# Performance work log

Measured on AMD Instinct MI355X. Metric: run time of the kernel, lower is better.

The kernel has to match this reference:

```python
import jax, jax.numpy as jnp
import numpy as np

POOL_K = {56: 8, 28: 4, 14: 2, 7: 1}


def _maxpool(x, k):
    # kernel == stride maxpool via reshape-max
    if k == 1:
        return x
    B, C, H, W = x.shape
    return x.reshape(B, C, H // k, k, W // k, k).max(axis=(3, 5))


def _scale(act):
    # act: [B, C, H0, W0] -> pooled [B, C, 7, 7]
    B, C, H0, W0 = act.shape
    p = _maxpool(act, POOL_K[H0]).reshape(B, C, -1)  # [B, C, HW], HW=49
    # heatmap[i,j,e,f] = sum_c p[i,c,e] * p[j,c,f]  -> [B, B, HW, HW]
    heat = jax.nn.softmax(jnp.einsum('ice,jcf->ijef', p, p), axis=-1)
    # out[i,j,e,c] = sum_f heat[i,j,e,f] * p[j,c,f]  -> [B, B, HW, C]
    out = jnp.einsum('ijef,jcf->ijec', heat, p)
    return out, heat


def setup_inputs() -> dict:
    key = jax.random.key(0)
    k1, k2, k3, k4 = jax.random.split(key, 4)
    B = 16
    return {
        'act1': jax.random.normal(k1, (B, 256, 56, 56), dtype=jnp.float32),
        'act2': jax.random.normal(k2, (B, 512, 28, 28), dtype=jnp.float32),
        'act3': jax.random.normal(k3, (B, 1024, 14, 14), dtype=jnp.float32),
        'act4': jax.random.normal(k4, (B, 2048, 7, 7), dtype=jnp.float32),
    }


def reference(act1, act2, act3, act4):
    outs_heats = [_scale(a) for a in (act1, act2, act3, act4)]
    outs = tuple(o for o, _ in outs_heats)
    heats = tuple(h for _, h in outs_heats)
    return outs + heats
```

## Files before the change

kernel.cpp:

```cpp
#include <hip/hip_runtime.h>
#include <hip/hip_bf16.h>
#include <cstdint>
#include <cstddef>


typedef __attribute__((ext_vector_type(8))) short s16x8;
typedef __attribute__((ext_vector_type(4))) float f32x4;
typedef __attribute__((ext_vector_type(4))) uint32_t u32x4;

#define SPART 802816

__device__ __forceinline__ unsigned short f2bf(float x) {
    uint32_t u = __float_as_uint(x);
    uint32_t r = (u + 0x7fff + ((u >> 16) & 1)) >> 16;
    return (unsigned short)r;
}
__device__ __forceinline__ float bf2f(unsigned short b) {
    return __uint_as_float(((uint32_t)b) << 16);
}
__device__ __forceinline__ void gll16(const void* g, void* l) {
    __builtin_amdgcn_global_load_lds(
        (const __attribute__((address_space(1))) uint32_t*)g,
        (__attribute__((address_space(3))) uint32_t*)l, 16, 0, 0);
}

struct PoolParams {
    const float* act[4];
    unsigned short* Pk[4];
    unsigned short* Vb[4];
    int C[4], H[4], k[4], G[4], cum[5];
};

__global__ __launch_bounds__(256) void pool_all_kernel(PoolParams pp) {
    __shared__ alignas(16) float plane[3136];
    int b = blockIdx.x, s = 0;
    while (b >= pp.cum[s + 1]) s++;
    const int rem = b - pp.cum[s];
    const int C = pp.C[s], H = pp.H[s], k = pp.k[s], G = pp.G[s];
    const int HW = H * H;
    const int nblk_c = C / G;
    const int i  = rem / nblk_c;
    const int c0 = (rem % nblk_c) * G;
    unsigned short* __restrict__ Pk = pp.Pk[s];
    unsigned short* __restrict__ Vb = pp.Vb[s];

    const float4* src4 = reinterpret_cast<const float4*>(pp.act[s] + ((size_t)i * C + c0) * HW);
    float4* plane4 = reinterpret_cast<float4*>(plane);
    for (int idx = threadIdx.x; idx < (G * HW) >> 2; idx += 256)
        plane4[idx] = src4[idx];
    __syncthreads();
    for (int idx = threadIdx.x; idx < G * 49; idx += 256) {
        const int e = idx / G, g = idx % G;
        const int eh = e / 7, ew = e % 7;
        const float* ppl = plane + g * HW + (eh * k) * H + ew * k;
        float m = -INFINITY;
        for (int dy = 0; dy < k; ++dy)
            for (int dx = 0; dx < k; ++dx)
                m = fmaxf(m, ppl[dy * H + dx]);
        const int c = c0 + g;
        const unsigned short hb = f2bf(m);
        const unsigned short lb = f2bf(m - bf2f(hb));
        const size_t pk = (((size_t)(c >> 2) * 896) + (size_t)i * 56 + e) * 8 + ((c & 3) * 2);
        *reinterpret_cast<uint32_t*>(&Pk[pk]) = (uint32_t)hb | ((uint32_t)lb << 16);
        const size_t vb = (((size_t)i * 8 + (e >> 3)) * C + c) * 8 + (e & 7);
        Vb[vb] = hb;
    }
    for (int idx = threadIdx.x; idx < 7 * G; idx += 256) {
        const int e = 49 + idx / G, g = idx % G, c = c0 + g;
        const size_t pk = (((size_t)(c >> 2) * 896) + (size_t)i * 56 + e) * 8 + ((c & 3) * 2);
        *reinterpret_cast<uint32_t*>(&Pk[pk]) = 0;
    }
    for (int idx = threadIdx.x; idx < 15 * G; idx += 256) {
        const int e = 49 + idx / G, g = idx % G, c = c0 + g;
        const size_t vb = (((size_t)i * 8 + (e >> 3)) * C + c) * 8 + (e & 7);
        Vb[vb] = 0;
    }
}

struct GramParams {
    const unsigned short* Pk[4];
    float* S[4];
    int Kblk[4];
    int cum[5];
};

__global__ __launch_bounds__(256) void gram_kernel(GramParams g) {
    __shared__ short lsA[4 * 128 * 8];
    __shared__ short lsB[4 * 128 * 8];
    int b = blockIdx.x, s = 0;
    while (b >= g.cum[s + 1]) s++;
    const int rem = b - g.cum[s];
    const int p = rem / 49, t = rem % 49;
    const int bi = t / 7, bj = t % 7;
    const int Kb = g.Kblk[s];
    const int kg0 = p * (Kb >> 3);
    const unsigned short* __restrict__ Pk = g.Pk[s];
    float* __restrict__ S = g.S[s] + (size_t)p * SPART;

    const int tid = threadIdx.x, lane = tid & 63, w = tid >> 6;
    const int wm = (w >> 1) * 64, wn = (w & 1) * 64;

    f32x4 acc[4][4];
    #pragma unroll
    for (int u = 0; u < 4; ++u)
        #pragma unroll
        for (int v = 0; v < 4; ++v)
            acc[u][v] = (f32x4){0.f, 0.f, 0.f, 0.f};

    const int half = lane >> 4, r16 = lane & 15;
    for (int it = 0; it < (Kb >> 5); ++it) {
        const int kq = kg0 + it * 4 + w;
        const char* ga = (const char*)Pk + ((size_t)kq * 896 + bi * 128) * 16 + lane * 16;
        const char* gb = (const char*)Pk + ((size_t)kq * 896 + bj * 128) * 16 + lane * 16;
        gll16(ga,        (char*)lsA + w * 2048);
        gll16(ga + 1024, (char*)lsA + w * 2048 + 1024);
        gll16(gb,        (char*)lsB + w * 2048);
        gll16(gb + 1024, (char*)lsB + w * 2048 + 1024);
        __syncthreads();
        s16x8 av[4], bv[4], cv[4];
        #pragma unroll
        for (int u = 0; u < 4; ++u) {
            av[u] = *reinterpret_cast<const s16x8*>(&lsA[((half * 128) + wm + 16 * u + r16) * 8]);
            union { u32x4 u4; s16x8 s8; } ub, uc;
            ub.u4 = *reinterpret_cast<const u32x4*>(&lsB[((half * 128) + wn + 16 * u + r16) * 8]);
            uc.u4 = (ub.u4 >> 16) | (ub.u4 << 16);
            bv[u] = ub.s8;
            cv[u] = uc.s8;
        }
        #pragma unroll
        for (int u = 0; u < 4; ++u)
            #pragma unroll
            for (int v = 0; v < 4; ++v) {
                acc[u][v] = __builtin_amdgcn_mfma_f32_16x16x32_bf16(av[u], bv[v], acc[u][v], 0, 0, 0);
                acc[u][v] = __builtin_amdgcn_mfma_f32_16x16x32_bf16(av[u], cv[v], acc[u][v], 0, 0, 0);
            }
        __syncthreads();
    }

    const int rowb = bi * 128 + wm + (lane >> 4) * 4;
    const int colb = bj * 128 + wn + (lane & 15);
    #pragma unroll
    for (int u = 0; u < 4; ++u)
        #pragma unroll
        for (int v = 0; v < 4; ++v)
            #pragma unroll
            for (int rg = 0; rg < 4; ++rg)
                S[(size_t)(rowb + 16 * u + rg) * 896 + colb + 16 * v] = acc[u][v][rg];
}

struct SoftParams {
    const float* S[4];
    float* heat[4];
    unsigned short* Hb[4];
    int np[4];
};

__global__ __launch_bounds__(256) void softmax_kernel(SoftParams sp) {
    const int grp = (blockIdx.x * 256 + threadIdx.x) >> 4;
    const int l = threadIdx.x & 15;
    const int s = grp / 12544;
    const int rem = grp % 12544;
    const int i = rem / 784;
    const int j = (rem / 49) % 16;
    const int e = rem % 49;
    const float* __restrict__ Sb = sp.S[s];
    const int np = sp.np[s];
    const size_t rowoff = ((size_t)(i * 56 + e)) * 896 + j * 56;

    float v[4];
    #pragma unroll
    for (int t = 0; t < 4; ++t) {
        const int f = l + t * 16;
        float x = -INFINITY;
        if (f < 49) {
            x = 0.f;
            for (int p = 0; p < np; ++p) x += Sb[(size_t)p * SPART + rowoff + f];
        }
        v[t] = x;
    }
    float m = fmaxf(fmaxf(v[0], v[1]), fmaxf(v[2], v[3]));
    #pragma unroll
    for (int d = 1; d < 16; d <<= 1) m = fmaxf(m, __shfl_xor(m, d, 16));
    float ex[4], sum = 0.f;
    #pragma unroll
    for (int t = 0; t < 4; ++t) {
        const int f = l + t * 16;
        ex[t] = (f < 49) ? __expf(v[t] - m) : 0.f;
        sum += ex[t];
    }
    #pragma unroll
    for (int d = 1; d < 16; d <<= 1) sum += __shfl_xor(sum, d, 16);
    const float inv = 1.f / sum;

    float* hrow = sp.heat[s] + (((size_t)(i * 16 + j)) * 49 + e) * 49;
    unsigned short* __restrict__ Hb = sp.Hb[s];
    const size_t hbrow = (size_t)i * 56 + e;
    #pragma unroll
    for (int t = 0; t < 4; ++t) {
        const int f = l + t * 16;
        const float hv = (f < 49) ? ex[t] * inv : 0.f;
        if (f < 49) hrow[f] = hv;
        Hb[(((size_t)j * 8 + (f >> 3)) * 896 + hbrow) * 8 + (f & 7)] = f2bf(hv);
    }
}

struct PvParams {
    const unsigned short* Hb[4];
    const unsigned short* Vb[4];
    float* out[4];
    int C[4];
    int cum[5];
};

__global__ __launch_bounds__(256) void pv_kernel(PvParams pv) {
    __shared__ short lsA[8 * 128 * 8];
    __shared__ short lsB[8 * 128 * 8];
    int b = blockIdx.x, s = 0;
    while (b >= pv.cum[s + 1]) s++;
    int rem = b - pv.cum[s];
    const int C = pv.C[s], nct = C >> 7;
    const int j  = rem / (nct * 2); rem %= nct * 2;
    const int ct = rem >> 1, rh = rem & 1;
    const int tid = threadIdx.x, lane = tid & 63, w = tid >> 6;
    const int wm = (w >> 1) * 64, wn = (w & 1) * 64;
    const unsigned short* __restrict__ Hb = pv.Hb[s];
    const unsigned short* __restrict__ Vb = pv.Vb[s];

    #pragma unroll
    for (int q = 0; q < 2; ++q) {
        const int kq = w + q * 4;
        const char* gb = (const char*)Vb + ((size_t)(j * 8 + kq) * C + ct * 128) * 16 + lane * 16;
        gll16(gb,        (char*)lsB + kq * 2048);
        gll16(gb + 1024, (char*)lsB + kq * 2048 + 1024);
    }

    const int r16 = lane & 15;
    for (int rt = rh; rt < 7; rt += 2) {
        #pragma unroll
        for (int q = 0; q < 2; ++q) {
            const int kq = w + q * 4;
            const char* ga = (const char*)Hb + ((size_t)(j * 8 + kq) * 896 + rt * 128) * 16 + lane * 16;
            gll16(ga,        (char*)lsA + kq * 2048);
            gll16(ga + 1024, (char*)lsA + kq * 2048 + 1024);
        }
        __syncthreads();

        f32x4 acc[4][4];
        #pragma unroll
        for (int u = 0; u < 4; ++u)
            #pragma unroll
            for (int v = 0; v < 4; ++v)
                acc[u][v] = (f32x4){0.f, 0.f, 0.f, 0.f};

        #pragma unroll
        for (int ks = 0; ks < 2; ++ks) {
            const int half = ks * 4 + (lane >> 4);
            s16x8 av[4], bv[4];
            #pragma unroll
            for (int u = 0; u < 4; ++u) {
                av[u] = *reinterpret_cast<const s16x8*>(&lsA[((half * 128) + wm + 16 * u + r16) * 8]);
                bv[u] = *reinterpret_cast<const s16x8*>(&lsB[((half * 128) + wn + 16 * u + r16) * 8]);
            }
            #pragma unroll
            for (int u = 0; u < 4; ++u)
                #pragma unroll
                for (int v = 0; v < 4; ++v)
                    acc[u][v] = __builtin_amdgcn_mfma_f32_16x16x32_bf16(av[u], bv[v], acc[u][v], 0, 0, 0);
        }

        #pragma unroll
        for (int u = 0; u < 4; ++u) {
            const int mb = rt * 128 + wm + 16 * u + (lane >> 4) * 4;
            #pragma unroll
            for (int rg = 0; rg < 4; ++rg) {
                const int mm = mb + rg;
                const int ii = mm / 56, e = mm % 56;
                if (e < 49) {
                    float* orow = pv.out[s] + (((size_t)(ii * 16 + j)) * 49 + e) * C + ct * 128 + (lane & 15);
                    #pragma unroll
                    for (int v = 0; v < 4; ++v)
                        orow[wn + 16 * v] = acc[u][v][rg];
                }
            }
        }
        __syncthreads();
    }
}

extern "C" void kernel_launch(void* const* d_in, const int* in_sizes, int n_in,
                              void* d_out, int out_size, void* d_ws, size_t ws_size,
                              hipStream_t stream) {
    const int Cs[4] = {256, 512, 1024, 2048};
    const int Hs[4] = {56, 28, 14, 7};
    const int ks[4] = {8, 4, 2, 1};
    const int Gs[4] = {1, 4, 16, 64};

    char* w0 = (char*)d_ws;
    size_t off = 0;
    unsigned short *Pk[4], *Vb[4], *Hb[4];
    for (int s = 0; s < 4; ++s) { Pk[s] = (unsigned short*)(w0 + off); off += (size_t)3584 * Cs[s]; }
    for (int s = 0; s < 4; ++s) { Vb[s] = (unsigned short*)(w0 + off); off += (size_t)2048 * Cs[s]; }
    for (int s = 0; s < 4; ++s) { Hb[s] = (unsigned short*)(w0 + off); off += (size_t)1835008; }

    int np[4] = {1, 2, 2, 4};
    {
        size_t need = off;
        for (int s = 0; s < 4; ++s) need += (size_t)np[s] * SPART * 4;
        if (ws_size < need) { np[0] = np[1] = np[2] = np[3] = 1; }
    }
    float* Sp[4];
    for (int s = 0; s < 4; ++s) { Sp[s] = (float*)(w0 + off); off += (size_t)np[s] * SPART * 4; }

    float* out = (float*)d_out;
    const size_t o1 = 0;
    const size_t o2 = o1 + (size_t)256 * 49 * 256;
    const size_t o3 = o2 + (size_t)256 * 49 * 512;
    const size_t o4 = o3 + (size_t)256 * 49 * 1024;
    const size_t h1 = o4 + (size_t)256 * 49 * 2048;
    const size_t h2 = h1 + (size_t)256 * 2401;
    const size_t h3 = h2 + (size_t)256 * 2401;
    const size_t h4 = h3 + (size_t)256 * 2401;
    float* heat[4] = {out + h1, out + h2, out + h3, out + h4};
    float* outs[4] = {out + o1, out + o2, out + o3, out + o4};

    PoolParams pp;
    pp.cum[0] = 0;
    for (int s = 0; s < 4; ++s) {
        pp.act[s] = (const float*)d_in[s];
        pp.Pk[s] = Pk[s]; pp.Vb[s] = Vb[s];
        pp.C[s] = Cs[s]; pp.H[s] = Hs[s]; pp.k[s] = ks[s]; pp.G[s] = Gs[s];
        pp.cum[s + 1] = pp.cum[s] + 16 * (Cs[s] / Gs[s]);
    }
    pool_all_kernel<<<pp.cum[4], 256, 0, stream>>>(pp);

    GramParams g;
    g.cum[0] = 0;
    for (int s = 0; s < 4; ++s) {
        g.Pk[s] = Pk[s];
        g.S[s] = Sp[s];
        g.Kblk[s] = 2 * Cs[s] / np[s];
        g.cum[s + 1] = g.cum[s] + np[s] * 49;
    }
    gram_kernel<<<g.cum[4], 256, 0, stream>>>(g);

    SoftParams sp;
    for (int s = 0; s < 4; ++s) {
        sp.S[s] = Sp[s]; sp.heat[s] = heat[s]; sp.Hb[s] = Hb[s]; sp.np[s] = np[s];
    }
    softmax_kernel<<<3136, 256, 0, stream>>>(sp);

    PvParams pv;
    pv.cum[0] = 0;
    for (int s = 0; s < 4; ++s) {
        pv.Hb[s] = Hb[s]; pv.Vb[s] = Vb[s]; pv.out[s] = outs[s]; pv.C[s] = Cs[s];
        pv.cum[s + 1] = pv.cum[s] + 16 * (Cs[s] >> 7) * 2;
    }
    pv_kernel<<<pv.cum[4], 256, 0, stream>>>(pv);
}
```

Before: 135.6 us.

## Double-buffer gram kernel LDS loads and split PV work per row tile

The gram kernel now double-buffers its LDS tiles, issuing the global-to-LDS load for the next K step before computing on the current one. This overlaps memory latency with MFMA work at the cost of twice the shared memory per block. The PV kernel gets one block per (j, row tile, column tile) instead of looping over row tiles inside a block. That raises the grid size and parallelism, but each Vb tile is now reloaded by every row-tile block.

```diff
diff --git a/kernel.cpp b/kernel.cpp
--- a/kernel.cpp
+++ b/kernel.cpp
@@ -85,8 +85,8 @@
 };
 
 __global__ __launch_bounds__(256) void gram_kernel(GramParams g) {
-    __shared__ short lsA[4 * 128 * 8];
-    __shared__ short lsB[4 * 128 * 8];
+    __shared__ short lsA[2][4096];
+    __shared__ short lsB[2][4096];
     int b = blockIdx.x, s = 0;
     while (b >= g.cum[s + 1]) s++;
     const int rem = b - g.cum[s];
@@ -108,21 +108,31 @@
             acc[u][v] = (f32x4){0.f, 0.f, 0.f, 0.f};
 
     const int half = lane >> 4, r16 = lane & 15;
-    for (int it = 0; it < (Kb >> 5); ++it) {
-        const int kq = kg0 + it * 4 + w;
-        const char* ga = (const char*)Pk + ((size_t)kq * 896 + bi * 128) * 16 + lane * 16;
-        const char* gb = (const char*)Pk + ((size_t)kq * 896 + bj * 128) * 16 + lane * 16;
-        gll16(ga,        (char*)lsA + w * 2048);
-        gll16(ga + 1024, (char*)lsA + w * 2048 + 1024);
-        gll16(gb,        (char*)lsB + w * 2048);
-        gll16(gb + 1024, (char*)lsB + w * 2048 + 1024);
-        __syncthreads();
+    const int nt = Kb >> 5;
+
+#define GSTAGE(buf, it) do {                                                        \
+        const int kq_ = kg0 + (it) * 4 + w;                                         \
+        const char* ga_ = (const char*)Pk + ((size_t)kq_ * 896 + bi * 128) * 16 + lane * 16; \
+        const char* gb_ = (const char*)Pk + ((size_t)kq_ * 896 + bj * 128) * 16 + lane * 16; \
+        gll16(ga_,        (char*)lsA[buf] + w * 2048);                              \
+        gll16(ga_ + 1024, (char*)lsA[buf] + w * 2048 + 1024);                       \
+        gll16(gb_,        (char*)lsB[buf] + w * 2048);                              \
+        gll16(gb_ + 1024, (char*)lsB[buf] + w * 2048 + 1024);                       \
+    } while (0)
+
+    GSTAGE(0, 0);
+    asm volatile("s_waitcnt vmcnt(0)" ::: "memory");
+    __builtin_amdgcn_s_barrier();
+
+    int cur = 0;
+    for (int it = 0; it < nt; ++it) {
+        if (it + 1 < nt) GSTAGE(cur ^ 1, it + 1);
         s16x8 av[4], bv[4], cv[4];
         #pragma unroll
         for (int u = 0; u < 4; ++u) {
-            av[u] = *reinterpret_cast<const s16x8*>(&lsA[((half * 128) + wm + 16 * u + r16) * 8]);
+            av[u] = *reinterpret_cast<const s16x8*>(&lsA[cur][((half * 128) + wm + 16 * u + r16) * 8]);
             union { u32x4 u4; s16x8 s8; } ub, uc;
-            ub.u4 = *reinterpret_cast<const u32x4*>(&lsB[((half * 128) + wn + 16 * u + r16) * 8]);
+            ub.u4 = *reinterpret_cast<const u32x4*>(&lsB[cur][((half * 128) + wn + 16 * u + r16) * 8]);
             uc.u4 = (ub.u4 >> 16) | (ub.u4 << 16);
             bv[u] = ub.s8;
             cv[u] = uc.s8;
@@ -134,8 +144,12 @@
                 acc[u][v] = __builtin_amdgcn_mfma_f32_16x16x32_bf16(av[u], bv[v], acc[u][v], 0, 0, 0);
                 acc[u][v] = __builtin_amdgcn_mfma_f32_16x16x32_bf16(av[u], cv[v], acc[u][v], 0, 0, 0);
             }
-        __syncthreads();
-    }
+        __builtin_amdgcn_sched_barrier(0);
+        asm volatile("s_waitcnt vmcnt(0)" ::: "memory");
+        __builtin_amdgcn_s_barrier();
+        cur ^= 1;
+    }
+#undef GSTAGE
 
     const int rowb = bi * 128 + wm + (lane >> 4) * 4;
     const int colb = bj * 128 + wn + (lane & 15);
@@ -219,8 +233,8 @@
     while (b >= pv.cum[s + 1]) s++;
     int rem = b - pv.cum[s];
     const int C = pv.C[s], nct = C >> 7;
-    const int j  = rem / (nct * 2); rem %= nct * 2;
-    const int ct = rem >> 1, rh = rem & 1;
+    const int j = rem / (7 * nct); rem %= 7 * nct;
+    const int rt = rem / nct, ct = rem % nct;
     const int tid = threadIdx.x, lane = tid & 63, w = tid >> 6;
     const int wm = (w >> 1) * 64, wn = (w & 1) * 64;
     const unsigned short* __restrict__ Hb = pv.Hb[s];
@@ -229,61 +243,53 @@
     #pragma unroll
     for (int q = 0; q < 2; ++q) {
         const int kq = w + q * 4;
+        const char* ga = (const char*)Hb + ((size_t)(j * 8 + kq) * 896 + rt * 128) * 16 + lane * 16;
         const char* gb = (const char*)Vb + ((size_t)(j * 8 + kq) * C + ct * 128) * 16 + lane * 16;
+        gll16(ga,        (char*)lsA + kq * 2048);
+        gll16(ga + 1024, (char*)lsA + kq * 2048 + 1024);
         gll16(gb,        (char*)lsB + kq * 2048);
         gll16(gb + 1024, (char*)lsB + kq * 2048 + 1024);
     }
+    __syncthreads();
+
+    f32x4 acc[4][4];
+    #pragma unroll
+    for (int u = 0; u < 4; ++u)
+        #pragma unroll
+        for (int v = 0; v < 4; ++v)
+            acc[u][v] = (f32x4){0.f, 0.f, 0.f, 0.f};
 
     const int r16 = lane & 15;
-    for (int rt = rh; rt < 7; rt += 2) {
-        #pragma unroll
-        for (int q = 0; q < 2; ++q) {
-            const int kq = w + q * 4;
-            const char* ga = (const char*)Hb + ((size_t)(j * 8 + kq) * 896 + rt * 128) * 16 + lane * 16;
-            gll16(ga,        (char*)lsA + kq * 2048);
-            gll16(ga + 1024, (char*)lsA + kq * 2048 + 1024);
+    #pragma unroll
+    for (int ks = 0; ks < 2; ++ks) {
+        const int half = ks * 4 + (lane >> 4);
+        s16x8 av[4], bv[4];
+        #pragma unroll
+        for (int u = 0; u < 4; ++u) {
+            av[u] = *reinterpret_cast<const s16x8*>(&lsA[((half * 128) + wm + 16 * u + r16) * 8]);
+            bv[u] = *reinterpret_cast<const s16x8*>(&lsB[((half * 128) + wn + 16 * u + r16) * 8]);
         }
-        __syncthreads();
-
-        f32x4 acc[4][4];
         #pragma unroll
         for (int u = 0; u < 4; ++u)
             #pragma unroll
             for (int v = 0; v < 4; ++v)
-                acc[u][v] = (f32x4){0.f, 0.f, 0.f, 0.f};
-
-        #pragma unroll
-        for (int ks = 0; ks < 2; ++ks) {
-            const int half = ks * 4 + (lane >> 4);
-            s16x8 av[4], bv[4];
-            #pragma unroll
-            for (int u = 0; u < 4; ++u) {
-                av[u] = *reinterpret_cast<const s16x8*>(&lsA[((half * 128) + wm + 16 * u + r16) * 8]);
-                bv[u] = *reinterpret_cast<const s16x8*>(&lsB[((half * 128) + wn + 16 * u + r16) * 8]);
-            }
-            #pragma unroll
-            for (int u = 0; u < 4; ++u)
+                acc[u][v] = __builtin_amdgcn_mfma_f32_16x16x32_bf16(av[u], bv[v], acc[u][v], 0, 0, 0);
+    }
+
+    #pragma unroll
+    for (int u = 0; u < 4; ++u) {
+        const int mb = rt * 128 + wm + 16 * u + (lane >> 4) * 4;
+        #pragma unroll
+        for (int rg = 0; rg < 4; ++rg) {
+            const int mm = mb + rg;
+            const int ii = mm / 56, e = mm % 56;
+            if (e < 49) {
+                float* orow = pv.out[s] + (((size_t)(ii * 16 + j)) * 49 + e) * C + ct * 128 + (lane & 15);
                 #pragma unroll
                 for (int v = 0; v < 4; ++v)
-                    acc[u][v] = __builtin_amdgcn_mfma_f32_16x16x32_bf16(av[u], bv[v], acc[u][v], 0, 0, 0);
-        }
-
-        #pragma unroll
-        for (int u = 0; u < 4; ++u) {
-            const int mb = rt * 128 + wm + 16 * u + (lane >> 4) * 4;
-            #pragma unroll
-            for (int rg = 0; rg < 4; ++rg) {
-                const int mm = mb + rg;
-                const int ii = mm / 56, e = mm % 56;
-                if (e < 49) {
-                    float* orow = pv.out[s] + (((size_t)(ii * 16 + j)) * 49 + e) * C + ct * 128 + (lane & 15);
-                    #pragma unroll
-                    for (int v = 0; v < 4; ++v)
-                        orow[wn + 16 * v] = acc[u][v][rg];
-                }
+                    orow[wn + 16 * v] = acc[u][v][rg];
             }
         }
-        __syncthreads();
     }
 }
 
@@ -353,7 +359,7 @@
     pv.cum[0] = 0;
     for (int s = 0; s < 4; ++s) {
         pv.Hb[s] = Hb[s]; pv.Vb[s] = Vb[s]; pv.out[s] = outs[s]; pv.C[s] = Cs[s];
-        pv.cum[s + 1] = pv.cum[s] + 16 * (Cs[s] >> 7) * 2;
+        pv.cum[s + 1] = pv.cum[s] + 16 * 7 * (Cs[s] >> 7);
     }
     pv_kernel<<<pv.cum[4], 256, 0, stream>>>(pv);
 }
```

Result: faster. 132.1 us (-2.6%).
